# Performance work log

Measured on AMD Instinct MI355X. Metric: run time of the kernel, lower is better.

Reference implementation:

```python
import jax, jax.numpy as jnp
import numpy as np

EPS = 1e-5
AVG_D = 32.0


def setup_inputs() -> dict:
    key = jax.random.key(0)
    ks = jax.random.split(key, 12)
    Ns, Nd, E, D, K = 1_000_000, 100_000, 3_200_000, 16, 2
    Fs, Fd, V = 4, 4, 100_000
    F = Fd + K  # predictor fields
    inp = {}
    inp["Cat_src"] = jax.random.randint(ks[0], (Ns, Fs), 0, V)
    inp["Cat_dst"] = jax.random.randint(ks[1], (Nd, Fd), 0, V)
    inp["src_ids"] = jax.random.randint(ks[2], (E,), 0, Ns)
    inp["dst_ids"] = jax.random.randint(ks[3], (E,), 0, Nd)
    inp["label"] = jax.random.randint(ks[4], (Nd,), 0, 2)
    inp["w"] = jax.random.normal(ks[5], (V, D), dtype=jnp.float32) * 0.05
    inp["W_agg"] = jax.random.normal(ks[6], (K, 12 * D, D), dtype=jnp.float32) * 0.05
    inp["b_agg"] = jnp.zeros((K, D), jnp.float32)
    inp["w_lin"] = jax.random.normal(ks[7], (F * D,), dtype=jnp.float32) * 0.05
    inp["b_lin"] = jnp.zeros((1,), jnp.float32)
    inp["W1"] = jax.random.normal(ks[8], (F * D, 64), dtype=jnp.float32) * 0.05
    inp["b1"] = jnp.zeros((64,), jnp.float32)
    inp["W2"] = jax.random.normal(ks[9], (64, 32), dtype=jnp.float32) * 0.05
    inp["b2"] = jnp.zeros((32,), jnp.float32)
    inp["W3"] = jax.random.normal(ks[10], (32, 1), dtype=jnp.float32) * 0.05
    inp["b3"] = jnp.zeros((1,), jnp.float32)
    return inp


def reference(Cat_src, Cat_dst, src_ids, dst_ids, label, w, W_agg, b_agg,
              w_lin, b_lin, W1, b1, W2, b2, W3, b3):
    Nd = Cat_dst.shape[0]
    # --- node embedding: gather cat fields, RowEmb with modes [mean, max] -> [Ns, K, D]
    emb = w[Cat_src]                                      # [Ns, Fs, D]
    h_src = jnp.stack([emb.mean(1), emb.max(1)], axis=1)  # [Ns, K, D]
    # --- multi-aggregator message passing (copy_u + segment min/max/mean, std via mean of h^2)
    m = h_src[src_ids]                                    # [E, K, D]
    deg = jax.ops.segment_sum(jnp.ones(src_ids.shape, m.dtype), dst_ids, Nd)
    safe = jnp.maximum(deg, 1.0)[:, None, None]
    mean = jax.ops.segment_sum(m, dst_ids, Nd) / safe
    mean2 = jax.ops.segment_sum(m * m, dst_ids, Nd) / safe
    has = (deg > 0)[:, None, None]
    mn = jnp.where(has, jax.ops.segment_min(m, dst_ids, Nd), 0.0)
    mx = jnp.where(has, jax.ops.segment_max(m, dst_ids, Nd), 0.0)
    std = jnp.sqrt(jax.nn.relu(mean2 - mean * mean) + EPS)
    tmp = jnp.concatenate([mean, mn, mx, std], axis=-1)   # [Nd, K, 4D]
    # --- PNA degree scalers: identity / amplification / attenuation
    logd = jnp.log(deg + 1.0)
    log_avg = jnp.log(AVG_D + 1.0)
    amp = (logd / log_avg)[:, None, None]
    att = jnp.where(logd > 0, log_avg / jnp.maximum(logd, EPS), 0.0)[:, None, None]
    scaled = jnp.concatenate([tmp, tmp * amp, tmp * att], axis=-1)  # [Nd, K, 12D]
    mes = jnp.einsum('nkf,kfd->nkd', scaled, W_agg) + b_agg          # [Nd, K, D]
    # --- final block: concat dst cat embeddings with aggregated messages
    x = jnp.concatenate([w[Cat_dst], mes], axis=1)        # [Nd, F, D]
    # --- DeepFM predictor: linear + FM pairwise + deep MLP
    flat = x.reshape(Nd, -1)
    lin = flat @ w_lin + b_lin[0]
    s = x.sum(1)
    fm = 0.5 * ((s * s) - (x * x).sum(1)).sum(-1)
    h = jax.nn.relu(flat @ W1 + b1)
    h = jax.nn.relu(h @ W2 + b2)
    deep = (h @ W3 + b3)[:, 0]
    pred = jax.nn.sigmoid(lin + fm + deep)
    return (pred, label)
```

## Files before the change

kernel.cpp:

```cpp
#include <hip/hip_runtime.h>
#include <math.h>

#define EPSF 1e-5f
#define CAP  88
#define SBH  9
#define MAXSB 256
#define SBCAP 23552
#define TILE 4096
#define SEG  8
#define XPADS2 104
#define X2PADS 72
#define NPACK 14336

typedef __attribute__((ext_vector_type(8))) short short8;
typedef __attribute__((ext_vector_type(4))) float float4v;

__device__ inline unsigned f2bf_rne(float x) {
    unsigned u = __float_as_uint(x);
    u += 0x7FFF + ((u >> 16) & 1);
    return u >> 16;
}
__device__ inline short bf16_of(float x) { return (short)f2bf_rne(x); }
__device__ inline float bf2f_lo(unsigned hv) { return __uint_as_float(hv << 16); }
__device__ inline float bf2f_hi(unsigned hv) { return __uint_as_float(hv & 0xFFFF0000u); }
__device__ inline float bf2f_s(ushort s) { return __uint_as_float((unsigned)s << 16); }

__global__ __launch_bounds__(256) void setup_all(
    int* sbcursor, int* deg, int Nd, int nsb,
    const float* __restrict__ W_agg, const float* __restrict__ W1,
    const float* __restrict__ W2, ushort* __restrict__ wpack,
    const float* __restrict__ w, ushort* __restrict__ wb, int VD, int do_cast)
{
    int nzc = (Nd + 255) >> 8;
    int bid = blockIdx.x;
    if (bid < nzc) {
        int i = bid * 256 + threadIdx.x;
        if (i < Nd) deg[i] = 0;
        if (bid == 0 && threadIdx.x < nsb) sbcursor[threadIdx.x] = threadIdx.x * SBCAP;
        return;
    }
    if (bid == nzc) {
        for (int it = threadIdx.x; it < 1792; it += 256) {
            if (it < 768) {
                int t_g = it >> 6; int rem = it & 63;
                int q = rem >> 4, col = rem & 15;
                int kvar = t_g / 6, t = t_g % 6;
                const float* src = W_agg + kvar * 3072 + (t * 32 + q * 8) * 16 + col;
                ushort* dst = wpack + (size_t)it * 8;
#pragma unroll
                for (int j = 0; j < 8; ++j) dst[j] = (ushort)f2bf_rne(src[j * 16]);
            } else if (it < 1536) {
                int i2 = it - 768;
                int t = i2 >> 8; int rem = i2 & 255;
                int q = rem >> 6, col = rem & 63;
                const float* src = W1 + (t * 32 + q * 8) * 64 + col;
                ushort* dst = wpack + 6144 + (size_t)i2 * 8;
#pragma unroll
                for (int j = 0; j < 8; ++j) dst[j] = (ushort)f2bf_rne(src[j * 64]);
            } else {
                int i2 = it - 1536;
                int t = i2 >> 7; int rem = i2 & 127;
                int q = rem >> 5, col = rem & 31;
                const float* src = W2 + (t * 32 + q * 8) * 32 + col;
                ushort* dst = wpack + 12288 + (size_t)i2 * 8;
#pragma unroll
                for (int j = 0; j < 8; ++j) dst[j] = (ushort)f2bf_rne(src[j * 32]);
            }
        }
        return;
    }
    if (!do_cast) return;
    int i4 = ((bid - nzc - 1) * 256 + threadIdx.x) * 4;
    if (i4 + 3 < VD) {
        float4 v = *(const float4*)(w + i4);
        ushort4 o;
        o.x = (ushort)f2bf_rne(v.x); o.y = (ushort)f2bf_rne(v.y);
        o.z = (ushort)f2bf_rne(v.z); o.w = (ushort)f2bf_rne(v.w);
        *(ushort4*)(wb + i4) = o;
    } else {
        for (int j = i4; j < VD; ++j) wb[j] = (ushort)f2bf_rne(w[j]);
    }
}

__global__ __launch_bounds__(256) void build_h(
    const int* __restrict__ Cat_src, const ushort* __restrict__ wb,
    unsigned* __restrict__ h, int Ns)
{
    int gid = blockIdx.x * 256 + threadIdx.x;
    int s = gid >> 4;
    if (s >= Ns) return;
    int lane = threadIdx.x & 63;
    int d = lane & 15;
    int c = Cat_src[s * 4 + (d & 3)];
    float vs = 0.f, vm = -INFINITY;
#pragma unroll
    for (int f = 0; f < 4; ++f) {
        int id = __shfl(c, (lane & 48) + f, 64);
        float a = bf2f_s(wb[id * 16 + d]);
        vs += a; vm = fmaxf(vm, a);
    }
    unsigned packed = f2bf_rne(vs * 0.25f) | (f2bf_rne(vm) << 16);
    __builtin_nontemporal_store(packed, &h[s * 16 + d]);
}

__global__ __launch_bounds__(256) void scatter_sb(
    const int* __restrict__ src_ids, const int* __restrict__ dst_ids,
    int* sbcursor, unsigned* __restrict__ pairs1, int E, int nsb)
{
    __shared__ int cnt[MAXSB];
    __shared__ int base[MAXSB];
    int tid = threadIdx.x;
    int t0 = blockIdx.x * TILE;
    for (int i = tid; i < nsb; i += 256) cnt[i] = 0;
    __syncthreads();
    int rank[TILE / 256];
#pragma unroll
    for (int j = 0; j < TILE / 256; ++j) {
        int e = t0 + j * 256 + tid;
        rank[j] = (e < E) ? atomicAdd(&cnt[dst_ids[e] >> SBH], 1) : 0;
    }
    __syncthreads();
    for (int i = tid; i < nsb; i += 256) {
        int c = cnt[i];
        base[i] = c ? atomicAdd(&sbcursor[i], c) : 0;
    }
    __syncthreads();
#pragma unroll
    for (int j = 0; j < TILE / 256; ++j) {
        int e = t0 + j * 256 + tid;
        if (e < E) {
            int d = dst_ids[e];
            int sb = d >> SBH;
            int idx = base[sb] + rank[j];
            if (idx < (sb + 1) * SBCAP)
                pairs1[idx] = ((unsigned)src_ids[e] << 9) | (unsigned)(d & 511);
        }
    }
}

__global__ __launch_bounds__(256) void scatter_fine3(
    const unsigned* __restrict__ pairs1, const int* __restrict__ sbcursor,
    unsigned* __restrict__ pairs2, int* __restrict__ deg, int Nd, int nsb,
    int nsbp)
{
    __shared__ int cnt[512];
    __shared__ int base[512];
    int S = blockIdx.x % nsbp, seg = blockIdx.x / nsbp;
    if (S >= nsb) return;
    int tid = threadIdx.x;
    int sbs = S * SBCAP;
    int sbe = sbcursor[S];
    if (sbe > sbs + SBCAP) sbe = sbs + SBCAP;
    int len = sbe - sbs;
    int per = (len + SEG - 1) / SEG;
    int s0 = sbs + seg * per;
    int s1 = s0 + per; if (s1 > sbe) s1 = sbe;
    cnt[tid] = 0; cnt[tid + 256] = 0;
    __syncthreads();
    int rank[12];
    unsigned pv[12];
    int nit = (s1 - s0 + 255) >> 8;
    if (nit > 12) nit = 12;
    for (int j = 0; j < nit; ++j) {
        int e = s0 + j * 256 + tid;
        if (e < s1) {
            unsigned p = __builtin_nontemporal_load(&pairs1[e]);
            pv[j] = p;
            rank[j] = atomicAdd(&cnt[p & 511u], 1);
        }
    }
    __syncthreads();
#pragma unroll
    for (int r = 0; r < 2; ++r) {
        int l = tid + r * 256;
        int c = cnt[l];
        int gdst = (S << 9) + l;
        base[l] = (c && gdst < Nd) ? atomicAdd(&deg[gdst], c) : 0;
    }
    __syncthreads();
    for (int j = 0; j < nit; ++j) {
        int e = s0 + j * 256 + tid;
        if (e < s1) {
            unsigned p = pv[j];
            int l = (int)(p & 511u);
            int idx = base[l] + rank[j];
            if (idx < CAP)
                pairs2[(size_t)((S << 9) + l) * CAP + idx] = p >> 9;
        }
    }
}

__device__ inline void emit_stats(float sum0, float sq0, float mn0, float mx0,
                                  float sum1, float sq1, float mn1, float mx1,
                                  int dg, int n, int lane, int sub,
                                  ushort* __restrict__ tmpb)
{
#pragma unroll
    for (int off = 16; off <= 32; off <<= 1) {
        sum0 += __shfl_xor(sum0, off); sq0 += __shfl_xor(sq0, off);
        mn0 = fminf(mn0, __shfl_xor(mn0, off)); mx0 = fmaxf(mx0, __shfl_xor(mx0, off));
        sum1 += __shfl_xor(sum1, off); sq1 += __shfl_xor(sq1, off);
        mn1 = fminf(mn1, __shfl_xor(mn1, off)); mx1 = fmaxf(mx1, __shfl_xor(mx1, off));
    }
    float safe = fmaxf((float)dg, 1.f);
    float r = 1.f / safe;
    bool has = dg > 0;
    float mean0 = sum0 * r, mean1 = sum1 * r;
    float sd0 = sqrtf(fmaxf(sq0 * r - mean0 * mean0, 0.f) + EPSF);
    float sd1 = sqrtf(fmaxf(sq1 * r - mean1 * mean1, 0.f) + EPSF);
    float v0 = (sub == 0) ? mean0 : (sub == 1) ? (has ? mn0 : 0.f)
             : (sub == 2) ? (has ? mx0 : 0.f) : sd0;
    float v1 = (sub == 0) ? mean1 : (sub == 1) ? (has ? mn1 : 0.f)
             : (sub == 2) ? (has ? mx1 : 0.f) : sd1;
    ushort* tp = tmpb + (size_t)n * 128;
    tp[lane] = (ushort)f2bf_rne(v0);
    tp[64 + lane] = (ushort)f2bf_rne(v1);
}

#define ACC8(HV)  do { \
    float me = bf2f_lo(HV); \
    float vm = bf2f_hi(HV); \
    sum0 += me; sq0 += me * me; \
    mn0 = fminf(mn0, me); mx0 = fmaxf(mx0, me); \
    sum1 += vm; sq1 += vm * vm; \
    mn1 = fminf(mn1, vm); mx1 = fmaxf(mx1, vm); } while (0)

__global__ __launch_bounds__(256) void agg_from_h2(
    const unsigned* __restrict__ h, const int* __restrict__ deg,
    const unsigned* __restrict__ pairs,
    ushort* __restrict__ tmpb, int Nd)
{
    int tid = threadIdx.x;
    int wv = tid >> 6, lane = tid & 63, sub = lane >> 4, d = lane & 15;
    int n = blockIdx.x * 4 + wv;
    if (n >= Nd) return;
    int dg = deg[n];
    int dgc = (dg < CAP) ? dg : CAP;
    const unsigned* pw = pairs + (size_t)n * CAP;

    float sum0 = 0.f, sq0 = 0.f, mn0 = INFINITY, mx0 = -INFINITY;
    float sum1 = 0.f, sq1 = 0.f, mn1 = INFINITY, mx1 = -INFINITY;

    int t64 = dgc >> 6;
    for (int t = 0; t < t64; ++t) {
        const unsigned* pp = pw + t * 64 + sub;
        unsigned pv[16], hv[16];
#pragma unroll
        for (int j = 0; j < 16; ++j) pv[j] = pp[j * 4];
#pragma unroll
        for (int j = 0; j < 16; ++j) hv[j] = h[pv[j] * 16 + d];
#pragma unroll
        for (int j = 0; j < 16; ++j) ACC8(hv[j]);
    }
    int base = t64 << 6;
    if (dgc & 32) {
        const unsigned* pp = pw + base + sub;
        unsigned pv[8], hv[8];
#pragma unroll
        for (int j = 0; j < 8; ++j) pv[j] = pp[j * 4];
#pragma unroll
        for (int j = 0; j < 8; ++j) hv[j] = h[pv[j] * 16 + d];
#pragma unroll
        for (int j = 0; j < 8; ++j) ACC8(hv[j]);
        base += 32;
    }
    int rem = dgc - base;
    if (rem > 0) {
        int last = dgc - 1;
        unsigned pv[8], hv[8];
#pragma unroll
        for (int j = 0; j < 8; ++j) {
            if (j * 4 < rem) {
                int e = base + j * 4 + sub;
                pv[j] = pw[e < last ? e : last];
            }
        }
#pragma unroll
        for (int j = 0; j < 8; ++j)
            if (j * 4 < rem) hv[j] = h[pv[j] * 16 + d];
#pragma unroll
        for (int j = 0; j < 8; ++j) {
            if (j * 4 < rem) {
                if (base + j * 4 + sub < dgc) ACC8(hv[j]);
            }
        }
    }
    emit_stats(sum0, sq0, mn0, mx0, sum1, sq1, mn1, mx1,
               dg, n, lane, sub, tmpb);
}

__global__ __launch_bounds__(256) void agg_from_w2(
    const int* __restrict__ Cat_src, const float* __restrict__ w,
    const ushort* __restrict__ wb, int use_bf,
    const int* __restrict__ deg, const unsigned* __restrict__ pairs,
    ushort* __restrict__ tmpb, int Nd)
{
    int tid = threadIdx.x;
    int wv = tid >> 6, lane = tid & 63, sub = lane >> 4, d = lane & 15;
    int n = blockIdx.x * 4 + wv;
    if (n >= Nd) return;
    int dg = deg[n];
    int dgc = (dg < CAP) ? dg : CAP;
    const unsigned* pw = pairs + (size_t)n * CAP;

    float sum0 = 0.f, sq0 = 0.f, mn0 = INFINITY, mx0 = -INFINITY;
    float sum1 = 0.f, sq1 = 0.f, mn1 = INFINITY, mx1 = -INFINITY;
    int nt = (dgc + 3) >> 2;
    for (int t = 0; t < nt; ++t) {
        int e4 = t * 4 + sub;
        int ec = (e4 < dgc) ? e4 : (dgc - 1);
        int src = (int)pw[ec];
        int cat = Cat_src[src * 4 + (d & 3)];
        float vs = 0.f, vm = -INFINITY;
        if (use_bf) {
#pragma unroll
            for (int f = 0; f < 4; ++f) {
                int id = __shfl(cat, sub * 16 + f, 64);
                float a = bf2f_s(wb[id * 16 + d]);
                vs += a; vm = fmaxf(vm, a);
            }
        } else {
#pragma unroll
            for (int f = 0; f < 4; ++f) {
                int id = __shfl(cat, sub * 16 + f, 64);
                float a = w[id * 16 + d];
                vs += a; vm = fmaxf(vm, a);
            }
        }
        if (e4 < dgc) {
            float me = vs * 0.25f;
            sum0 += me; sq0 += me * me;
            mn0 = fminf(mn0, me); mx0 = fmaxf(mx0, me);
            sum1 += vm; sq1 += vm * vm;
            mn1 = fminf(mn1, vm); mx1 = fmaxf(mx1, vm);
        }
    }
    emit_stats(sum0, sq0, mn0, mx0, sum1, sq1, mn1, mx1,
               dg, n, lane, sub, tmpb);
}

__global__ __launch_bounds__(256) void finalize_mfma(
    const int* __restrict__ Cat_dst, const int* __restrict__ label,
    const float* __restrict__ w, const ushort* __restrict__ wpack,
    const float* __restrict__ b_agg,
    const float* __restrict__ w_lin, const float* __restrict__ b_lin,
    const float* __restrict__ b1, const float* __restrict__ b2,
    const float* __restrict__ W3, const float* __restrict__ b3,
    const int* __restrict__ deg_arr, const ushort* __restrict__ tmpb,
    float* __restrict__ out, int Nd)
{
    __shared__ __align__(16) ushort sx[4][16 * XPADS2];
    __shared__ __align__(16) ushort sx2[4][16 * X2PADS];
    __shared__ float sdeep[4][16];

    int tid = threadIdx.x;
    int wv = tid >> 6, lane = tid & 63;
    int q = lane >> 4, m = lane & 15;
    int n0 = (blockIdx.x * 4 + wv) * 16;
    int n = n0 + m;
    int nc = (n < Nd) ? n : (Nd - 1);

    ushort* X = sx[wv];
    ushort* X2 = sx2[wv];

    float fdeg = (float)deg_arr[nc];
    float logd = logf(fdeg + 1.f);
    const float logavg = logf(33.0f);
    float amp = logd / logavg;
    float att = (logd > 0.f) ? (logavg / fmaxf(logd, EPSF)) : 0.f;
    float ampr[4], attr[4];
#pragma unroll
    for (int r = 0; r < 4; ++r) {
        ampr[r] = __shfl(amp, q * 4 + r, 64);
        attr[r] = __shfl(att, q * 4 + r, 64);
    }

    const ushort* tpn = tmpb + (size_t)nc * 128;
#pragma unroll
    for (int kvar = 0; kvar < 2; ++kvar) {
        short8 af0 = *(const short8*)(tpn + kvar * 64 + q * 8);
        short8 af1 = *(const short8*)(tpn + kvar * 64 + 32 + q * 8);
        float4v aI = {0.f,0.f,0.f,0.f}, aA = {0.f,0.f,0.f,0.f}, aT = {0.f,0.f,0.f,0.f};
#pragma unroll
        for (int sb = 0; sb < 3; ++sb) {
            short8 b0 = *(const short8*)(wpack +
                (size_t)(((kvar * 6 + sb * 2) * 4 + q) * 16 + m) * 8);
            short8 b1v = *(const short8*)(wpack +
                (size_t)(((kvar * 6 + sb * 2 + 1) * 4 + q) * 16 + m) * 8);
            if (sb == 0) {
                aI = __builtin_amdgcn_mfma_f32_16x16x32_bf16(af0, b0, aI, 0, 0, 0);
                aI = __builtin_amdgcn_mfma_f32_16x16x32_bf16(af1, b1v, aI, 0, 0, 0);
            } else if (sb == 1) {
                aA = __builtin_amdgcn_mfma_f32_16x16x32_bf16(af0, b0, aA, 0, 0, 0);
                aA = __builtin_amdgcn_mfma_f32_16x16x32_bf16(af1, b1v, aA, 0, 0, 0);
            } else {
                aT = __builtin_amdgcn_mfma_f32_16x16x32_bf16(af0, b0, aT, 0, 0, 0);
                aT = __builtin_amdgcn_mfma_f32_16x16x32_bf16(af1, b1v, aT, 0, 0, 0);
            }
        }
        float bias = b_agg[kvar * 16 + m];
#pragma unroll
        for (int r = 0; r < 4; ++r)
            X[(q * 4 + r) * XPADS2 + 64 + kvar * 16 + m] = (ushort)f2bf_rne(
                aI[r] + ampr[r] * aA[r] + attr[r] * aT[r] + bias);
    }
    {
        int nl = lane >> 2, fl = lane & 3;
        int nn = n0 + nl;
        int nnc = (nn < Nd) ? nn : (Nd - 1);
        int cid = Cat_dst[nnc * 4 + fl];
        const float4* R = (const float4*)(w + (size_t)cid * 16);
        float4 r0 = R[0], r1 = R[1], r2 = R[2], r3 = R[3];
        short8 o0, o1;
        o0[0] = bf16_of(r0.x); o0[1] = bf16_of(r0.y);
        o0[2] = bf16_of(r0.z); o0[3] = bf16_of(r0.w);
        o0[4] = bf16_of(r1.x); o0[5] = bf16_of(r1.y);
        o0[6] = bf16_of(r1.z); o0[7] = bf16_of(r1.w);
        o1[0] = bf16_of(r2.x); o1[1] = bf16_of(r2.y);
        o1[2] = bf16_of(r2.z); o1[3] = bf16_of(r2.w);
        o1[4] = bf16_of(r3.x); o1[5] = bf16_of(r3.y);
        o1[6] = bf16_of(r3.z); o1[7] = bf16_of(r3.w);
        ushort* xp = X + nl * XPADS2 + fl * 16;
        *(short8*)(xp) = o0;
        *(short8*)(xp + 8) = o1;
    }
    __syncthreads();

    float lin = 0.f, sq = 0.f;
    float sd[16];
#pragma unroll
    for (int u = 0; u < 16; ++u) sd[u] = 0.f;
    {
        const ushort* xp = X + m * XPADS2 + q * 16;
        const float* wl = w_lin + q * 16;
#pragma unroll
        for (int u = 0; u < 16; ++u) {
            float v = bf2f_s(xp[u]);
            lin += v * wl[u]; sq += v * v; sd[u] += v;
        }
    }
    if (q < 2) {
        const ushort* xp = X + m * XPADS2 + (4 + q) * 16;
        const float* wl = w_lin + (4 + q) * 16;
#pragma unroll
        for (int u = 0; u < 16; ++u) {
            float v = bf2f_s(xp[u]);
            lin += v * wl[u]; sq += v * v; sd[u] += v;
        }
    }
#pragma unroll
    for (int off = 16; off <= 32; off <<= 1) {
        lin += __shfl_xor(lin, off);
        sq  += __shfl_xor(sq, off);
#pragma unroll
        for (int u = 0; u < 16; ++u) sd[u] += __shfl_xor(sd[u], off);
    }
    float fm = 0.f;
#pragma unroll
    for (int u = 0; u < 16; ++u) fm += sd[u] * sd[u];
    fm = 0.5f * (fm - sq);

    short8 xa[3];
#pragma unroll
    for (int t = 0; t < 3; ++t)
        xa[t] = *(const short8*)(X + m * XPADS2 + t * 32 + q * 8);
#pragma unroll
    for (int nt = 0; nt < 4; ++nt) {
        float4v acc = {0.f, 0.f, 0.f, 0.f};
#pragma unroll
        for (int t = 0; t < 3; ++t) {
            short8 bf = *(const short8*)(wpack + 6144 +
                (size_t)((t * 4 + q) * 64 + nt * 16 + m) * 8);
            acc = __builtin_amdgcn_mfma_f32_16x16x32_bf16(xa[t], bf, acc, 0, 0, 0);
        }
        float bb = b1[nt * 16 + m];
#pragma unroll
        for (int r = 0; r < 4; ++r)
            X2[(q * 4 + r) * X2PADS + nt * 16 + m] =
                (ushort)f2bf_rne(fmaxf(acc[r] + bb, 0.f));
    }
    __syncthreads();

    short8 ha[2];
#pragma unroll
    for (int t = 0; t < 2; ++t)
        ha[t] = *(const short8*)(X2 + m * X2PADS + t * 32 + q * 8);
    float dp[4] = {0.f, 0.f, 0.f, 0.f};
#pragma unroll
    for (int nt = 0; nt < 2; ++nt) {
        float4v acc = {0.f, 0.f, 0.f, 0.f};
#pragma unroll
        for (int t = 0; t < 2; ++t) {
            short8 bf = *(const short8*)(wpack + 12288 +
                (size_t)((t * 4 + q) * 32 + nt * 16 + m) * 8);
            acc = __builtin_amdgcn_mfma_f32_16x16x32_bf16(ha[t], bf, acc, 0, 0, 0);
        }
        float bb = b2[nt * 16 + m];
        float w3 = W3[nt * 16 + m];
#pragma unroll
        for (int r = 0; r < 4; ++r)
            dp[r] += fmaxf(acc[r] + bb, 0.f) * w3;
    }
#pragma unroll
    for (int off = 1; off <= 8; off <<= 1) {
#pragma unroll
        for (int r = 0; r < 4; ++r) dp[r] += __shfl_xor(dp[r], off);
    }
    if (m < 4)
        sdeep[wv][q * 4 + m] = (m == 0) ? dp[0] : (m == 1) ? dp[1]
                             : (m == 2) ? dp[2] : dp[3];
    __syncthreads();
    float deep = sdeep[wv][m];

    if (q == 0 && n < Nd) {
        float z = lin + b_lin[0] + fm + deep + b3[0];
        float pred = 1.f / (1.f + expf(-z));
        out[n] = pred;
        out[Nd + n] = (float)label[n];
    }
}

extern "C" void kernel_launch(void* const* d_in, const int* in_sizes, int n_in,
                              void* d_out, int out_size, void* d_ws, size_t ws_size,
                              hipStream_t stream) {
    const int*   Cat_src = (const int*)d_in[0];
    const int*   Cat_dst = (const int*)d_in[1];
    const int*   src_ids = (const int*)d_in[2];
    const int*   dst_ids = (const int*)d_in[3];
    const int*   label   = (const int*)d_in[4];
    const float* w       = (const float*)d_in[5];
    const float* W_agg   = (const float*)d_in[6];
    const float* b_agg   = (const float*)d_in[7];
    const float* w_lin   = (const float*)d_in[8];
    const float* b_lin   = (const float*)d_in[9];
    const float* W1      = (const float*)d_in[10];
    const float* b1      = (const float*)d_in[11];
    const float* W2      = (const float*)d_in[12];
    const float* b2      = (const float*)d_in[13];
    const float* W3      = (const float*)d_in[14];
    const float* b3      = (const float*)d_in[15];

    int E  = in_sizes[2];
    int Nd = in_sizes[4];
    int Ns = in_sizes[0] / 4;
    int VD = in_sizes[5];
    int nsb = (Nd + (1 << SBH) - 1) >> SBH;
    int nsbp = (nsb + 7) & ~7;

    int* sbcursor = (int*)d_ws;
    int* deg      = sbcursor + MAXSB;
    size_t off_p2 = (((size_t)(MAXSB + Nd)) * 4 + 255) & ~(size_t)255;
    unsigned* pairs2 = (unsigned*)((char*)d_ws + off_p2);
    size_t off_u = (off_p2 + (size_t)Nd * CAP * 4 + 255) & ~(size_t)255;
    unsigned* pairs1 = (unsigned*)((char*)d_ws + off_u);
    ushort*   tmpb   = (ushort*)((char*)d_ws + off_u);
    size_t u_p1 = (size_t)nsb * SBCAP * 4;
    size_t u_tm = (size_t)Nd * 256;
    size_t u_bytes = (u_p1 > u_tm) ? u_p1 : u_tm;
    size_t off_w = (off_u + u_bytes + 255) & ~(size_t)255;
    ushort* wpack  = (ushort*)((char*)d_ws + off_w);
    ushort* w_bf16 = wpack + NPACK;
    unsigned* h    = (unsigned*)(w_bf16 + VD);

    size_t need_common = off_w + (size_t)NPACK * 2;
    size_t need_A = need_common + (size_t)VD * 2;
    size_t need_B = need_A + (size_t)Ns * 64;
    int mode = (ws_size >= need_B) ? 2 : (ws_size >= need_A) ? 1 : 0;

    float* out = (float*)d_out;

    int nzc = (Nd + 255) >> 8;
    int ncb = (mode >= 1) ? (VD / 4 + 255) / 256 : 0;
    hipLaunchKernelGGL(setup_all, dim3(nzc + 1 + ncb), dim3(256), 0, stream,
                       sbcursor, deg, Nd, nsb, W_agg, W1, W2, wpack,
                       w, w_bf16, VD, mode >= 1);
    if (mode == 2) {
        int hb = (int)(((size_t)Ns * 16 + 255) / 256);
        hipLaunchKernelGGL(build_h, dim3(hb), dim3(256), 0, stream,
                           Cat_src, w_bf16, h, Ns);
    }
    hipLaunchKernelGGL(scatter_sb, dim3((E + TILE - 1) / TILE), dim3(256), 0, stream,
                       src_ids, dst_ids, sbcursor, pairs1, E, nsb);
    hipLaunchKernelGGL(scatter_fine3, dim3(nsbp * SEG), dim3(256), 0, stream,
                       pairs1, sbcursor, pairs2, deg, Nd, nsb, nsbp);
    int nab = (Nd + 3) >> 2;
    if (mode == 2) {
        hipLaunchKernelGGL(agg_from_h2, dim3(nab), dim3(256), 0, stream,
                           h, deg, pairs2, tmpb, Nd);
    } else {
        hipLaunchKernelGGL(agg_from_w2, dim3(nab), dim3(256), 0, stream,
                           Cat_src, w, w_bf16, mode, deg, pairs2, tmpb, Nd);
    }
    hipLaunchKernelGGL(finalize_mfma, dim3((Nd + 63) / 64), dim3(256), 0, stream,
                       Cat_dst, label, w, wpack, b_agg, w_lin, b_lin,
                       b1, b2, W3, b3, deg, tmpb, out, Nd);
}
```

Before: 316.7 us.

## Fuse aggregation into finalize kernel and merge h-build into prep kernel

New measurement: 353.7 us. +11.7%, slower.

```diff
diff --git a/kernel.cpp b/kernel.cpp
--- a/kernel.cpp
+++ b/kernel.cpp
@@ -10,6 +10,7 @@
 #define SEG  8
 #define XPADS2 104
 #define X2PADS 72
+#define TPAD 136
 #define NPACK 14336
 
 typedef __attribute__((ext_vector_type(8))) short short8;
@@ -25,11 +26,13 @@
 __device__ inline float bf2f_hi(unsigned hv) { return __uint_as_float(hv & 0xFFFF0000u); }
 __device__ inline float bf2f_s(ushort s) { return __uint_as_float((unsigned)s << 16); }
 
-__global__ __launch_bounds__(256) void setup_all(
+__global__ __launch_bounds__(256) void prep_all(
     int* sbcursor, int* deg, int Nd, int nsb,
     const float* __restrict__ W_agg, const float* __restrict__ W1,
     const float* __restrict__ W2, ushort* __restrict__ wpack,
-    const float* __restrict__ w, ushort* __restrict__ wb, int VD, int do_cast)
+    const float* __restrict__ w, ushort* __restrict__ wb, int VD,
+    const int* __restrict__ Cat_src, unsigned* __restrict__ h, int Ns,
+    int ncb, int do_h)
 {
     int nzc = (Nd + 255) >> 8;
     int bid = blockIdx.x;
@@ -69,24 +72,21 @@
         }
         return;
     }
-    if (!do_cast) return;
-    int i4 = ((bid - nzc - 1) * 256 + threadIdx.x) * 4;
-    if (i4 + 3 < VD) {
-        float4 v = *(const float4*)(w + i4);
-        ushort4 o;
-        o.x = (ushort)f2bf_rne(v.x); o.y = (ushort)f2bf_rne(v.y);
-        o.z = (ushort)f2bf_rne(v.z); o.w = (ushort)f2bf_rne(v.w);
-        *(ushort4*)(wb + i4) = o;
-    } else {
-        for (int j = i4; j < VD; ++j) wb[j] = (ushort)f2bf_rne(w[j]);
-    }
-}
-
-__global__ __launch_bounds__(256) void build_h(
-    const int* __restrict__ Cat_src, const ushort* __restrict__ wb,
-    unsigned* __restrict__ h, int Ns)
-{
-    int gid = blockIdx.x * 256 + threadIdx.x;
+    if (bid < nzc + 1 + ncb) {
+        int i4 = ((bid - nzc - 1) * 256 + threadIdx.x) * 4;
+        if (i4 + 3 < VD) {
+            float4 v = *(const float4*)(w + i4);
+            ushort4 o;
+            o.x = (ushort)f2bf_rne(v.x); o.y = (ushort)f2bf_rne(v.y);
+            o.z = (ushort)f2bf_rne(v.z); o.w = (ushort)f2bf_rne(v.w);
+            *(ushort4*)(wb + i4) = o;
+        } else {
+            for (int j = i4; j < VD; ++j) wb[j] = (ushort)f2bf_rne(w[j]);
+        }
+        return;
+    }
+    if (!do_h) return;
+    int gid = (bid - nzc - 1 - ncb) * 256 + threadIdx.x;
     int s = gid >> 4;
     if (s >= Ns) return;
     int lane = threadIdx.x & 63;
@@ -96,7 +96,7 @@
 #pragma unroll
     for (int f = 0; f < 4; ++f) {
         int id = __shfl(c, (lane & 48) + f, 64);
-        float a = bf2f_s(wb[id * 16 + d]);
+        float a = w[id * 16 + d];
         vs += a; vm = fmaxf(vm, a);
     }
     unsigned packed = f2bf_rne(vs * 0.25f) | (f2bf_rne(vm) << 16);
@@ -192,8 +192,8 @@
 
 __device__ inline void emit_stats(float sum0, float sq0, float mn0, float mx0,
                                   float sum1, float sq1, float mn1, float mx1,
-                                  int dg, int n, int lane, int sub,
-                                  ushort* __restrict__ tmpb)
+                                  int dg, int lane, int sub,
+                                  ushort* __restrict__ tp)
 {
 #pragma unroll
     for (int off = 16; off <= 32; off <<= 1) {
@@ -212,7 +212,6 @@
              : (sub == 2) ? (has ? mx0 : 0.f) : sd0;
     float v1 = (sub == 0) ? mean1 : (sub == 1) ? (has ? mn1 : 0.f)
              : (sub == 2) ? (has ? mx1 : 0.f) : sd1;
-    ushort* tp = tmpb + (size_t)n * 128;
     tp[lane] = (ushort)f2bf_rne(v0);
     tp[64 + lane] = (ushort)f2bf_rne(v1);
 }
@@ -225,143 +224,76 @@
     sum1 += vm; sq1 += vm * vm; \
     mn1 = fminf(mn1, vm); mx1 = fmaxf(mx1, vm); } while (0)
 
-__global__ __launch_bounds__(256) void agg_from_h2(
-    const unsigned* __restrict__ h, const int* __restrict__ deg,
+__global__ __launch_bounds__(256) void agg_finalize(
+    const unsigned* __restrict__ h, const int* __restrict__ deg_arr,
     const unsigned* __restrict__ pairs,
-    ushort* __restrict__ tmpb, int Nd)
-{
-    int tid = threadIdx.x;
-    int wv = tid >> 6, lane = tid & 63, sub = lane >> 4, d = lane & 15;
-    int n = blockIdx.x * 4 + wv;
-    if (n >= Nd) return;
-    int dg = deg[n];
-    int dgc = (dg < CAP) ? dg : CAP;
-    const unsigned* pw = pairs + (size_t)n * CAP;
-
-    float sum0 = 0.f, sq0 = 0.f, mn0 = INFINITY, mx0 = -INFINITY;
-    float sum1 = 0.f, sq1 = 0.f, mn1 = INFINITY, mx1 = -INFINITY;
-
-    int t64 = dgc >> 6;
-    for (int t = 0; t < t64; ++t) {
-        const unsigned* pp = pw + t * 64 + sub;
-        unsigned pv[16], hv[16];
-#pragma unroll
-        for (int j = 0; j < 16; ++j) pv[j] = pp[j * 4];
-#pragma unroll
-        for (int j = 0; j < 16; ++j) hv[j] = h[pv[j] * 16 + d];
-#pragma unroll
-        for (int j = 0; j < 16; ++j) ACC8(hv[j]);
-    }
-    int base = t64 << 6;
-    if (dgc & 32) {
-        const unsigned* pp = pw + base + sub;
-        unsigned pv[8], hv[8];
-#pragma unroll
-        for (int j = 0; j < 8; ++j) pv[j] = pp[j * 4];
-#pragma unroll
-        for (int j = 0; j < 8; ++j) hv[j] = h[pv[j] * 16 + d];
-#pragma unroll
-        for (int j = 0; j < 8; ++j) ACC8(hv[j]);
-        base += 32;
-    }
-    int rem = dgc - base;
-    if (rem > 0) {
-        int last = dgc - 1;
-        unsigned pv[8], hv[8];
-#pragma unroll
-        for (int j = 0; j < 8; ++j) {
-            if (j * 4 < rem) {
-                int e = base + j * 4 + sub;
-                pv[j] = pw[e < last ? e : last];
-            }
-        }
-#pragma unroll
-        for (int j = 0; j < 8; ++j)
-            if (j * 4 < rem) hv[j] = h[pv[j] * 16 + d];
-#pragma unroll
-        for (int j = 0; j < 8; ++j) {
-            if (j * 4 < rem) {
-                if (base + j * 4 + sub < dgc) ACC8(hv[j]);
-            }
-        }
-    }
-    emit_stats(sum0, sq0, mn0, mx0, sum1, sq1, mn1, mx1,
-               dg, n, lane, sub, tmpb);
-}
-
-__global__ __launch_bounds__(256) void agg_from_w2(
-    const int* __restrict__ Cat_src, const float* __restrict__ w,
-    const ushort* __restrict__ wb, int use_bf,
-    const int* __restrict__ deg, const unsigned* __restrict__ pairs,
-    ushort* __restrict__ tmpb, int Nd)
-{
-    int tid = threadIdx.x;
-    int wv = tid >> 6, lane = tid & 63, sub = lane >> 4, d = lane & 15;
-    int n = blockIdx.x * 4 + wv;
-    if (n >= Nd) return;
-    int dg = deg[n];
-    int dgc = (dg < CAP) ? dg : CAP;
-    const unsigned* pw = pairs + (size_t)n * CAP;
-
-    float sum0 = 0.f, sq0 = 0.f, mn0 = INFINITY, mx0 = -INFINITY;
-    float sum1 = 0.f, sq1 = 0.f, mn1 = INFINITY, mx1 = -INFINITY;
-    int nt = (dgc + 3) >> 2;
-    for (int t = 0; t < nt; ++t) {
-        int e4 = t * 4 + sub;
-        int ec = (e4 < dgc) ? e4 : (dgc - 1);
-        int src = (int)pw[ec];
-        int cat = Cat_src[src * 4 + (d & 3)];
-        float vs = 0.f, vm = -INFINITY;
-        if (use_bf) {
-#pragma unroll
-            for (int f = 0; f < 4; ++f) {
-                int id = __shfl(cat, sub * 16 + f, 64);
-                float a = bf2f_s(wb[id * 16 + d]);
-                vs += a; vm = fmaxf(vm, a);
-            }
-        } else {
-#pragma unroll
-            for (int f = 0; f < 4; ++f) {
-                int id = __shfl(cat, sub * 16 + f, 64);
-                float a = w[id * 16 + d];
-                vs += a; vm = fmaxf(vm, a);
-            }
-        }
-        if (e4 < dgc) {
-            float me = vs * 0.25f;
-            sum0 += me; sq0 += me * me;
-            mn0 = fminf(mn0, me); mx0 = fmaxf(mx0, me);
-            sum1 += vm; sq1 += vm * vm;
-            mn1 = fminf(mn1, vm); mx1 = fmaxf(mx1, vm);
-        }
-    }
-    emit_stats(sum0, sq0, mn0, mx0, sum1, sq1, mn1, mx1,
-               dg, n, lane, sub, tmpb);
-}
-
-__global__ __launch_bounds__(256) void finalize_mfma(
     const int* __restrict__ Cat_dst, const int* __restrict__ label,
     const float* __restrict__ w, const ushort* __restrict__ wpack,
     const float* __restrict__ b_agg,
     const float* __restrict__ w_lin, const float* __restrict__ b_lin,
     const float* __restrict__ b1, const float* __restrict__ b2,
     const float* __restrict__ W3, const float* __restrict__ b3,
-    const int* __restrict__ deg_arr, const ushort* __restrict__ tmpb,
     float* __restrict__ out, int Nd)
 {
     __shared__ __align__(16) ushort sx[4][16 * XPADS2];
-    __shared__ __align__(16) ushort sx2[4][16 * X2PADS];
-    __shared__ float sdeep[4][16];
+    __shared__ __align__(16) ushort uni[4][16 * TPAD];
 
     int tid = threadIdx.x;
     int wv = tid >> 6, lane = tid & 63;
     int q = lane >> 4, m = lane & 15;
-    int n0 = (blockIdx.x * 4 + wv) * 16;
+    int n0 = blockIdx.x * 64 + wv * 16;
+    ushort* X = sx[wv];
+    ushort* stmp = uni[wv];
+
+    for (int it = 0; it < 16; ++it) {
+        int n = n0 + it;
+        int dg = (n < Nd) ? deg_arr[n] : 0;
+        int dgc = (dg < CAP) ? dg : CAP;
+        const unsigned* pw = pairs + (size_t)((n < Nd) ? n : 0) * CAP;
+
+        float sum0 = 0.f, sq0 = 0.f, mn0 = INFINITY, mx0 = -INFINITY;
+        float sum1 = 0.f, sq1 = 0.f, mn1 = INFINITY, mx1 = -INFINITY;
+
+        int nfull = dgc >> 5;
+        for (int t = 0; t < nfull; ++t) {
+            const unsigned* pp = pw + t * 32 + q;
+            unsigned pv[8], hv[8];
+#pragma unroll
+            for (int j = 0; j < 8; ++j) pv[j] = pp[j * 4];
+#pragma unroll
+            for (int j = 0; j < 8; ++j) hv[j] = h[pv[j] * 16 + m];
+#pragma unroll
+            for (int j = 0; j < 8; ++j) ACC8(hv[j]);
+        }
+        int base = nfull << 5;
+        int rem = dgc - base;
+        if (rem > 0) {
+            int last = dgc - 1;
+            unsigned pv[8], hv[8];
+#pragma unroll
+            for (int j = 0; j < 8; ++j) {
+                if (j * 4 < rem) {
+                    int e = base + j * 4 + q;
+                    pv[j] = pw[e < last ? e : last];
+                }
+            }
+#pragma unroll
+            for (int j = 0; j < 8; ++j)
+                if (j * 4 < rem) hv[j] = h[pv[j] * 16 + m];
+#pragma unroll
+            for (int j = 0; j < 8; ++j) {
+                if (j * 4 < rem) {
+                    if (base + j * 4 + q < dgc) ACC8(hv[j]);
+                }
+            }
+        }
+        emit_stats(sum0, sq0, mn0, mx0, sum1, sq1, mn1, mx1,
+                   dg, lane, q, stmp + it * TPAD);
+    }
+    __syncthreads();
+
     int n = n0 + m;
     int nc = (n < Nd) ? n : (Nd - 1);
-
-    ushort* X = sx[wv];
-    ushort* X2 = sx2[wv];
 
     float fdeg = (float)deg_arr[nc];
     float logd = logf(fdeg + 1.f);
@@ -375,7 +307,7 @@
         attr[r] = __shfl(att, q * 4 + r, 64);
     }
 
-    const ushort* tpn = tmpb + (size_t)nc * 128;
+    const ushort* tpn = stmp + m * TPAD;
 #pragma unroll
     for (int kvar = 0; kvar < 2; ++kvar) {
         short8 af0 = *(const short8*)(tpn + kvar * 64 + q * 8);
@@ -426,6 +358,240 @@
     }
     __syncthreads();
 
+    ushort* X2 = uni[wv];
+    float* sdeep = (float*)(uni[wv] + 16 * X2PADS);
+
+    float lin = 0.f, sq = 0.f;
+    float sd[16];
+#pragma unroll
+    for (int u = 0; u < 16; ++u) sd[u] = 0.f;
+    {
+        const ushort* xp = X + m * XPADS2 + q * 16;
+        const float* wl = w_lin + q * 16;
+#pragma unroll
+        for (int u = 0; u < 16; ++u) {
+            float v = bf2f_s(xp[u]);
+            lin += v * wl[u]; sq += v * v; sd[u] += v;
+        }
+    }
+    if (q < 2) {
+        const ushort* xp = X + m * XPADS2 + (4 + q) * 16;
+        const float* wl = w_lin + (4 + q) * 16;
+#pragma unroll
+        for (int u = 0; u < 16; ++u) {
+            float v = bf2f_s(xp[u]);
+            lin += v * wl[u]; sq += v * v; sd[u] += v;
+        }
+    }
+#pragma unroll
+    for (int off = 16; off <= 32; off <<= 1) {
+        lin += __shfl_xor(lin, off);
+        sq  += __shfl_xor(sq, off);
+#pragma unroll
+        for (int u = 0; u < 16; ++u) sd[u] += __shfl_xor(sd[u], off);
+    }
+    float fm = 0.f;
+#pragma unroll
+    for (int u = 0; u < 16; ++u) fm += sd[u] * sd[u];
+    fm = 0.5f * (fm - sq);
+
+    short8 xa[3];
+#pragma unroll
+    for (int t = 0; t < 3; ++t)
+        xa[t] = *(const short8*)(X + m * XPADS2 + t * 32 + q * 8);
+#pragma unroll
+    for (int nt = 0; nt < 4; ++nt) {
+        float4v acc = {0.f, 0.f, 0.f, 0.f};
+#pragma unroll
+        for (int t = 0; t < 3; ++t) {
+            short8 bf = *(const short8*)(wpack + 6144 +
+                (size_t)((t * 4 + q) * 64 + nt * 16 + m) * 8);
+            acc = __builtin_amdgcn_mfma_f32_16x16x32_bf16(xa[t], bf, acc, 0, 0, 0);
+        }
+        float bb = b1[nt * 16 + m];
+#pragma unroll
+        for (int r = 0; r < 4; ++r)
+            X2[(q * 4 + r) * X2PADS + nt * 16 + m] =
+                (ushort)f2bf_rne(fmaxf(acc[r] + bb, 0.f));
+    }
+    __syncthreads();
+
+    short8 ha[2];
+#pragma unroll
+    for (int t = 0; t < 2; ++t)
+        ha[t] = *(const short8*)(X2 + m * X2PADS + t * 32 + q * 8);
+    float dp[4] = {0.f, 0.f, 0.f, 0.f};
+#pragma unroll
+    for (int nt = 0; nt < 2; ++nt) {
+        float4v acc = {0.f, 0.f, 0.f, 0.f};
+#pragma unroll
+        for (int t = 0; t < 2; ++t) {
+            short8 bf = *(const short8*)(wpack + 12288 +
+                (size_t)((t * 4 + q) * 32 + nt * 16 + m) * 8);
+            acc = __builtin_amdgcn_mfma_f32_16x16x32_bf16(ha[t], bf, acc, 0, 0, 0);
+        }
+        float bb = b2[nt * 16 + m];
+        float w3 = W3[nt * 16 + m];
+#pragma unroll
+        for (int r = 0; r < 4; ++r)
+            dp[r] += fmaxf(acc[r] + bb, 0.f) * w3;
+    }
+#pragma unroll
+    for (int off = 1; off <= 8; off <<= 1) {
+#pragma unroll
+        for (int r = 0; r < 4; ++r) dp[r] += __shfl_xor(dp[r], off);
+    }
+    if (m < 4)
+        sdeep[q * 4 + m] = (m == 0) ? dp[0] : (m == 1) ? dp[1]
+                         : (m == 2) ? dp[2] : dp[3];
+    __syncthreads();
+    float deep = sdeep[m];
+
+    if (q == 0 && n < Nd) {
+        float z = lin + b_lin[0] + fm + deep + b3[0];
+        float pred = 1.f / (1.f + expf(-z));
+        out[n] = pred;
+        out[Nd + n] = (float)label[n];
+    }
+}
+
+__global__ __launch_bounds__(256) void agg_from_w2(
+    const int* __restrict__ Cat_src, const float* __restrict__ w,
+    const ushort* __restrict__ wb, int use_bf,
+    const int* __restrict__ deg, const unsigned* __restrict__ pairs,
+    ushort* __restrict__ tmpb, int Nd)
+{
+    int tid = threadIdx.x;
+    int wv = tid >> 6, lane = tid & 63, sub = lane >> 4, d = lane & 15;
+    int n = blockIdx.x * 4 + wv;
+    if (n >= Nd) return;
+    int dg = deg[n];
+    int dgc = (dg < CAP) ? dg : CAP;
+    const unsigned* pw = pairs + (size_t)n * CAP;
+
+    float sum0 = 0.f, sq0 = 0.f, mn0 = INFINITY, mx0 = -INFINITY;
+    float sum1 = 0.f, sq1 = 0.f, mn1 = INFINITY, mx1 = -INFINITY;
+    int nt = (dgc + 3) >> 2;
+    for (int t = 0; t < nt; ++t) {
+        int e4 = t * 4 + sub;
+        int ec = (e4 < dgc) ? e4 : (dgc - 1);
+        int src = (int)pw[ec];
+        int cat = Cat_src[src * 4 + (d & 3)];
+        float vs = 0.f, vm = -INFINITY;
+        if (use_bf) {
+#pragma unroll
+            for (int f = 0; f < 4; ++f) {
+                int id = __shfl(cat, sub * 16 + f, 64);
+                float a = bf2f_s(wb[id * 16 + d]);
+                vs += a; vm = fmaxf(vm, a);
+            }
+        } else {
+#pragma unroll
+            for (int f = 0; f < 4; ++f) {
+                int id = __shfl(cat, sub * 16 + f, 64);
+                float a = w[id * 16 + d];
+                vs += a; vm = fmaxf(vm, a);
+            }
+        }
+        if (e4 < dgc) {
+            float me = vs * 0.25f;
+            sum0 += me; sq0 += me * me;
+            mn0 = fminf(mn0, me); mx0 = fmaxf(mx0, me);
+            sum1 += vm; sq1 += vm * vm;
+            mn1 = fminf(mn1, vm); mx1 = fmaxf(mx1, vm);
+        }
+    }
+    emit_stats(sum0, sq0, mn0, mx0, sum1, sq1, mn1, mx1,
+               dg, lane, sub, tmpb + (size_t)n * 128);
+}
+
+__global__ __launch_bounds__(256) void finalize_mfma(
+    const int* __restrict__ Cat_dst, const int* __restrict__ label,
+    const float* __restrict__ w, const ushort* __restrict__ wpack,
+    const float* __restrict__ b_agg,
+    const float* __restrict__ w_lin, const float* __restrict__ b_lin,
+    const float* __restrict__ b1, const float* __restrict__ b2,
+    const float* __restrict__ W3, const float* __restrict__ b3,
+    const int* __restrict__ deg_arr, const ushort* __restrict__ tmpb,
+    float* __restrict__ out, int Nd)
+{
+    __shared__ __align__(16) ushort sx[4][16 * XPADS2];
+    __shared__ __align__(16) ushort sx2[4][16 * X2PADS];
+    __shared__ float sdeep[4][16];
+
+    int tid = threadIdx.x;
+    int wv = tid >> 6, lane = tid & 63;
+    int q = lane >> 4, m = lane & 15;
+    int n0 = (blockIdx.x * 4 + wv) * 16;
+    int n = n0 + m;
+    int nc = (n < Nd) ? n : (Nd - 1);
+
+    ushort* X = sx[wv];
+    ushort* X2 = sx2[wv];
+
+    float fdeg = (float)deg_arr[nc];
+    float logd = logf(fdeg + 1.f);
+    const float logavg = logf(33.0f);
+    float amp = logd / logavg;
+    float att = (logd > 0.f) ? (logavg / fmaxf(logd, EPSF)) : 0.f;
+    float ampr[4], attr[4];
+#pragma unroll
+    for (int r = 0; r < 4; ++r) {
+        ampr[r] = __shfl(amp, q * 4 + r, 64);
+        attr[r] = __shfl(att, q * 4 + r, 64);
+    }
+
+    const ushort* tpn = tmpb + (size_t)nc * 128;
+#pragma unroll
+    for (int kvar = 0; kvar < 2; ++kvar) {
+        short8 af0 = *(const short8*)(tpn + kvar * 64 + q * 8);
+        short8 af1 = *(const short8*)(tpn + kvar * 64 + 32 + q * 8);
+        float4v aI = {0.f,0.f,0.f,0.f}, aA = {0.f,0.f,0.f,0.f}, aT = {0.f,0.f,0.f,0.f};
+#pragma unroll
+        for (int sb = 0; sb < 3; ++sb) {
+            short8 b0 = *(const short8*)(wpack +
+                (size_t)(((kvar * 6 + sb * 2) * 4 + q) * 16 + m) * 8);
+            short8 b1v = *(const short8*)(wpack +
+                (size_t)(((kvar * 6 + sb * 2 + 1) * 4 + q) * 16 + m) * 8);
+            if (sb == 0) {
+                aI = __builtin_amdgcn_mfma_f32_16x16x32_bf16(af0, b0, aI, 0, 0, 0);
+                aI = __builtin_amdgcn_mfma_f32_16x16x32_bf16(af1, b1v, aI, 0, 0, 0);
+            } else if (sb == 1) {
+                aA = __builtin_amdgcn_mfma_f32_16x16x32_bf16(af0, b0, aA, 0, 0, 0);
+                aA = __builtin_amdgcn_mfma_f32_16x16x32_bf16(af1, b1v, aA, 0, 0, 0);
+            } else {
+                aT = __builtin_amdgcn_mfma_f32_16x16x32_bf16(af0, b0, aT, 0, 0, 0);
+                aT = __builtin_amdgcn_mfma_f32_16x16x32_bf16(af1, b1v, aT, 0, 0, 0);
+            }
+        }
+        float bias = b_agg[kvar * 16 + m];
+#pragma unroll
+        for (int r = 0; r < 4; ++r)
+            X[(q * 4 + r) * XPADS2 + 64 + kvar * 16 + m] = (ushort)f2bf_rne(
+                aI[r] + ampr[r] * aA[r] + attr[r] * aT[r] + bias);
+    }
+    {
+        int nl = lane >> 2, fl = lane & 3;
+        int nn = n0 + nl;
+        int nnc = (nn < Nd) ? nn : (Nd - 1);
+        int cid = Cat_dst[nnc * 4 + fl];
+        const float4* R = (const float4*)(w + (size_t)cid * 16);
+        float4 r0 = R[0], r1 = R[1], r2 = R[2], r3 = R[3];
+        short8 o0, o1;
+        o0[0] = bf16_of(r0.x); o0[1] = bf16_of(r0.y);
+        o0[2] = bf16_of(r0.z); o0[3] = bf16_of(r0.w);
+        o0[4] = bf16_of(r1.x); o0[5] = bf16_of(r1.y);
+        o0[6] = bf16_of(r1.z); o0[7] = bf16_of(r1.w);
+        o1[0] = bf16_of(r2.x); o1[1] = bf16_of(r2.y);
+        o1[2] = bf16_of(r2.z); o1[3] = bf16_of(r2.w);
+        o1[4] = bf16_of(r3.x); o1[5] = bf16_of(r3.y);
+        o1[6] = bf16_of(r3.z); o1[7] = bf16_of(r3.w);
+        ushort* xp = X + nl * XPADS2 + fl * 16;
+        *(short8*)(xp) = o0;
+        *(short8*)(xp + 8) = o1;
+    }
+    __syncthreads();
+
     float lin = 0.f, sq = 0.f;
     float sd[16];
 #pragma unroll
@@ -570,28 +736,25 @@
     float* out = (float*)d_out;
 
     int nzc = (Nd + 255) >> 8;
-    int ncb = (mode >= 1) ? (VD / 4 + 255) / 256 : 0;
-    hipLaunchKernelGGL(setup_all, dim3(nzc + 1 + ncb), dim3(256), 0, stream,
+    int ncb = (mode == 1) ? (VD / 4 + 255) / 256 : 0;
+    int hb  = (mode == 2) ? (int)(((size_t)Ns * 16 + 255) / 256) : 0;
+    hipLaunchKernelGGL(prep_all, dim3(nzc + 1 + ncb + hb), dim3(256), 0, stream,
                        sbcursor, deg, Nd, nsb, W_agg, W1, W2, wpack,
-                       w, w_bf16, VD, mode >= 1);
-    if (mode == 2) {
-        int hb = (int)(((size_t)Ns * 16 + 255) / 256);
-        hipLaunchKernelGGL(build_h, dim3(hb), dim3(256), 0, stream,
-                           Cat_src, w_bf16, h, Ns);
-    }
+                       w, w_bf16, VD, Cat_src, h, Ns, ncb, mode == 2);
     hipLaunchKernelGGL(scatter_sb, dim3((E + TILE - 1) / TILE), dim3(256), 0, stream,
                        src_ids, dst_ids, sbcursor, pairs1, E, nsb);
     hipLaunchKernelGGL(scatter_fine3, dim3(nsbp * SEG), dim3(256), 0, stream,
                        pairs1, sbcursor, pairs2, deg, Nd, nsb, nsbp);
-    int nab = (Nd + 3) >> 2;
     if (mode == 2) {
-        hipLaunchKernelGGL(agg_from_h2, dim3(nab), dim3(256), 0, stream,
-                           h, deg, pairs2, tmpb, Nd);
+        hipLaunchKernelGGL(agg_finalize, dim3((Nd + 63) / 64), dim3(256), 0, stream,
+                           h, deg, pairs2, Cat_dst, label, w, wpack, b_agg,
+                           w_lin, b_lin, b1, b2, W3, b3, out, Nd);
     } else {
+        int nab = (Nd + 3) >> 2;
         hipLaunchKernelGGL(agg_from_w2, dim3(nab), dim3(256), 0, stream,
                            Cat_src, w, w_bf16, mode, deg, pairs2, tmpb, Nd);
-    }
-    hipLaunchKernelGGL(finalize_mfma, dim3((Nd + 63) / 64), dim3(256), 0, stream,
-                       Cat_dst, label, w, wpack, b_agg, w_lin, b_lin,
-                       b1, b2, W3, b3, deg, tmpb, out, Nd);
-}
+        hipLaunchKernelGGL(finalize_mfma, dim3((Nd + 63) / 64), dim3(256), 0, stream,
+                           Cat_dst, label, w, wpack, b_agg, w_lin, b_lin,
+                           b1, b2, W3, b3, deg, tmpb, out, Nd);
+    }
+}
```
